# Optimization experiments

Hardware: AMD Instinct MI355X
Metric: run time of the kernel (lower is better)

## Reference

```python
import jax, jax.numpy as jnp
import numpy as np

N_NODES = 50000


def gcn_conv(x, W, b, src, dst, ew, n_nodes):
    """PyG GCNConv: out = D^{-1/2}(A + I)D^{-1/2} (x @ W) + b, A weighted by ew.

    Self loops (weight 1) are handled analytically instead of appending edges.
    """
    h = x @ W  # [N, out]
    # degree includes self-loop weight of 1
    deg = jax.ops.segment_sum(ew, dst, num_segments=n_nodes) + 1.0  # [N]
    dinv = jnp.where(deg > 0, jax.lax.rsqrt(deg), 0.0)
    norm = dinv[src] * ew * dinv[dst]  # [E]
    # message = norm * h[src], scatter-add to dst
    agg = jax.ops.segment_sum(h[src] * norm[:, None], dst, num_segments=n_nodes)
    # self-loop contribution: dinv[i] * 1 * dinv[i] * h[i]
    agg = agg + h * (dinv * dinv)[:, None]
    return agg + b


def setup_inputs() -> dict:
    key = jax.random.key(0)
    k = jax.random.split(key, 8)
    n, e, d_in, d_h = N_NODES, 600000, 128, 128
    x = jax.random.normal(k[0], (n, d_in), dtype=jnp.float32)
    edge_index = jax.random.randint(k[1], (2, e), 0, n, dtype=jnp.int64)
    edge_attr = jax.random.uniform(k[2], (e,), dtype=jnp.float32)
    s1 = 1.0 / np.sqrt(d_in)
    s2 = 1.0 / np.sqrt(d_h)
    W1 = jax.random.uniform(k[3], (d_in, d_h), jnp.float32, -s1, s1)
    b1 = jnp.zeros((d_h,), jnp.float32)
    W2 = jax.random.uniform(k[4], (d_h, d_h), jnp.float32, -s2, s2)
    b2 = jnp.zeros((d_h,), jnp.float32)
    return {"x": x, "edge_index": edge_index, "edge_attr": edge_attr,
            "W1": W1, "b1": b1, "W2": W2, "b2": b2}


def reference(x, edge_index, edge_attr, W1, b1, W2, b2):
    src, dst = edge_index[0], edge_index[1]
    h = gcn_conv(x, W1, b1, src, dst, edge_attr, N_NODES)
    h = jax.nn.relu(h)
    # dropout is identity in eval mode (deterministic reference)
    out = gcn_conv(h, W2, b2, src, dst, edge_attr, N_NODES)
    return out
```

## Files before the change

kernel.cpp:

```cpp
#include <hip/hip_runtime.h>
#include <stdint.h>

#define D 128
#define EPB2 1024
#define CSZ 128

typedef __bf16 bf16x8 __attribute__((ext_vector_type(8)));
typedef float f32x4 __attribute__((ext_vector_type(4)));

__device__ inline float bf2f(unsigned short u) {
    return __uint_as_float((unsigned)u << 16);
}
__device__ inline unsigned short f2bf(float f) {
    unsigned u = __float_as_uint(f);
    return (unsigned short)((u + 0x7FFF + ((u >> 16) & 1)) >> 16);
}

struct Params {
    const float* x; const int* ei; const float* ew;
    const float* W1; const float* b1; const float* W2; const float* b2;
    float* out;
    int N, E, C, B2n, gb, hb;
    unsigned short *Wt1, *Wt2;
    unsigned int* ctot; int* cbase; unsigned int* gcur;
    float* dinv; int* cnt; int* rowstart;
    int2* brec; int2* erec;
    unsigned short *Hbuf, *H2;
};


__device__ inline void dev_prep(int which, const Params& p) {
    const float* W = (which == 0) ? p.W1 : p.W2;
    unsigned short* Wt = (which == 0) ? p.Wt1 : p.Wt2;
    for (int i = threadIdx.x; i < 2048; i += 256) {
        int nn = i >> 4;
        int kc = (i & 15) << 3;
        ushort4 o0, o1;
        o0.x = f2bf(W[(kc + 0) * 128 + nn]); o0.y = f2bf(W[(kc + 1) * 128 + nn]);
        o0.z = f2bf(W[(kc + 2) * 128 + nn]); o0.w = f2bf(W[(kc + 3) * 128 + nn]);
        o1.x = f2bf(W[(kc + 4) * 128 + nn]); o1.y = f2bf(W[(kc + 5) * 128 + nn]);
        o1.z = f2bf(W[(kc + 6) * 128 + nn]); o1.w = f2bf(W[(kc + 7) * 128 + nn]);
        *(ushort4*)(Wt + nn * 128 + kc) = o0;
        *(ushort4*)(Wt + nn * 128 + kc + 4) = o1;
    }
}

__device__ inline void dev_hist2(int b, const Params& p, unsigned int* hist) {
    for (int i = threadIdx.x; i < p.C; i += 256) hist[i] = 0;
    __syncthreads();
    const int base = b * EPB2 + threadIdx.x;
#pragma unroll
    for (int k = 0; k < EPB2 / 256; ++k) {
        int e = base + k * 256;
        if (e < p.E) atomicAdd(&hist[((unsigned)p.ei[p.E + e]) >> 7], 1u);
    }
    __syncthreads();
    for (int i = threadIdx.x; i < p.C; i += 256) {
        unsigned v = hist[i];
        if (v) atomicAdd(&p.ctot[i], v);
    }
}

__device__ inline void dev_cscan(const Params& p, int* s) {
    const int tid = threadIdx.x;
    const int c0 = tid, c1 = tid + 256;
    s[c0] = (c0 < p.C) ? (int)p.ctot[c0] : 0;
    s[c1] = (c1 < p.C) ? (int)p.ctot[c1] : 0;
    __syncthreads();
    for (int off = 1; off < 512; off <<= 1) {
        int t0 = (c0 >= off) ? s[c0 - off] : 0;
        int t1 = (c1 >= off) ? s[c1 - off] : 0;
        __syncthreads();
        s[c0] += t0; s[c1] += t1;
        __syncthreads();
    }
    if (c0 < p.C) { int b0 = (c0 == 0) ? 0 : s[c0 - 1]; p.cbase[c0] = b0; p.gcur[c0] = (unsigned)b0; }
    if (c1 < p.C) { int b1 = s[c1 - 1]; p.cbase[c1] = b1; p.gcur[c1] = (unsigned)b1; }
    if (tid == 0) p.cbase[p.C] = p.E;
}

__device__ inline void dev_scat2(int b, const Params& p, unsigned int* a) {
    unsigned int* hcnt = a;
    unsigned int* hcur = a + 512;
    const int tid = threadIdx.x;
    for (int i = tid; i < p.C; i += 256) hcnt[i] = 0;
    __syncthreads();
    const int base = b * EPB2 + tid;
#pragma unroll
    for (int k = 0; k < EPB2 / 256; ++k) {
        int e = base + k * 256;
        if (e < p.E) atomicAdd(&hcnt[((unsigned)p.ei[p.E + e]) >> 7], 1u);
    }
    __syncthreads();
    for (int i = tid; i < p.C; i += 256) {
        unsigned c = hcnt[i];
        hcur[i] = c ? atomicAdd(&p.gcur[i], c) : 0u;
    }
    __syncthreads();
#pragma unroll
    for (int k = 0; k < EPB2 / 256; ++k) {
        int e = base + k * 256;
        if (e < p.E) {
            int s = p.ei[e];
            unsigned d = (unsigned)p.ei[p.E + e];
            float w = p.ew[e];
            int c = (int)(d >> 7);
            unsigned r = atomicAdd(&hcur[c], 1u);
            p.brec[r] = make_int2((int)((d << 16) | (unsigned)s), __float_as_int(w));
        }
    }
}

__device__ inline void dev_cbuild(int c, const Params& p, unsigned int* a, int cs, int ce) {
    unsigned int* hcnt = a;
    unsigned int* hdeg = a + CSZ;
    unsigned int* lsc  = a + 2 * CSZ;
    unsigned int* curs = a + 3 * CSZ;
    const int tid = threadIdx.x;
    if (tid < CSZ) { hcnt[tid] = 0; hdeg[tid] = 0; }
    __syncthreads();
    for (int i = cs + tid; i < ce; i += 256) {
        int2 r = p.brec[i];
        int local = (int)(((unsigned)r.x) >> 16) & (CSZ - 1);
        atomicAdd(&hcnt[local], 1u);
        atomicAdd(&hdeg[local], (unsigned)(__int_as_float(r.y) * 16777216.0f));
    }
    __syncthreads();
    if (tid < CSZ) lsc[tid] = hcnt[tid];
    __syncthreads();
    for (int off = 1; off < CSZ; off <<= 1) {
        unsigned t = (tid < CSZ && tid >= off) ? lsc[tid - off] : 0u;
        __syncthreads();
        if (tid < CSZ) lsc[tid] += t;
        __syncthreads();
    }
    if (tid < CSZ) {
        unsigned excl = lsc[tid] - hcnt[tid];
        curs[tid] = excl;
        int node = c * CSZ + tid;
        if (node < p.N) {
            p.rowstart[node] = cs + (int)excl;
            p.cnt[node] = (int)hcnt[tid];
            float deg = 1.0f + (float)hdeg[tid] * (1.0f / 16777216.0f);
            p.dinv[node] = rsqrtf(deg);
        }
    }
    __syncthreads();
    for (int i = cs + tid; i < ce; i += 256) {
        int2 r = p.brec[i];
        int local = (int)(((unsigned)r.x) >> 16) & (CSZ - 1);
        unsigned rk = atomicAdd(&curs[local], 1u);
        p.erec[cs + (int)rk] = make_int2(r.x & 0xFFFF, r.y);
    }
}

template <bool IN_BF16>
__device__ inline void mfma_body(unsigned short* sE,
                                 const void* __restrict__ Xv,
                                 const unsigned short* __restrict__ Wt,
                                 unsigned short* __restrict__ H, int n, int blk) {
    const int tid = threadIdx.x;
    const int row0 = blk * 64;
    const int lane = tid & 63;
    const int wv = tid >> 6;
    const int qm = lane & 15;
    const int quad = lane >> 4;

    const int arow = row0 + wv * 16 + qm;
    const int ar = (arow < n) ? arow : (n - 1);

    f32x4 acc[8];
#pragma unroll
    for (int i = 0; i < 8; ++i) acc[i] = (f32x4){0.f, 0.f, 0.f, 0.f};

#pragma unroll
    for (int kb = 0; kb < 4; ++kb) {
        const int koff = kb * 32 + quad * 8;
        bf16x8 a;
        if (IN_BF16) {
            a = *(const bf16x8*)((const unsigned short*)Xv + (size_t)ar * 128 + koff);
        } else {
            const float* Xf = (const float*)Xv + (size_t)ar * 128 + koff;
            float4 v0 = *(const float4*)(Xf);
            float4 v1 = *(const float4*)(Xf + 4);
            union { bf16x8 v; ushort4 u[2]; } cv;
            cv.u[0].x = f2bf(v0.x); cv.u[0].y = f2bf(v0.y);
            cv.u[0].z = f2bf(v0.z); cv.u[0].w = f2bf(v0.w);
            cv.u[1].x = f2bf(v1.x); cv.u[1].y = f2bf(v1.y);
            cv.u[1].z = f2bf(v1.z); cv.u[1].w = f2bf(v1.w);
            a = cv.v;
        }
#pragma unroll
        for (int n0 = 0; n0 < 8; ++n0) {
            bf16x8 b = *(const bf16x8*)(Wt + (n0 * 16 + qm) * 128 + koff);
            acc[n0] = __builtin_amdgcn_mfma_f32_16x16x32_bf16(a, b, acc[n0], 0, 0, 0);
        }
    }

#pragma unroll
    for (int n0 = 0; n0 < 8; ++n0)
#pragma unroll
        for (int r = 0; r < 4; ++r)
            sE[(wv * 16 + quad * 4 + r) * 136 + n0 * 16 + qm] = f2bf(acc[n0][r]);
    __syncthreads();

    const int row_in = lane >> 2;
    const int c0 = (lane & 3) * 4;
    const int grow = row0 + wv * 16 + row_in;
    if (grow < n) {
#pragma unroll
        for (int j = 0; j < 4; ++j)
            *(int4*)(H + (size_t)grow * 128 + (c0 + j) * 8) =
                *(const int4*)(&sE[(wv * 16 + row_in) * 136 + (c0 + j) * 8]);
    }
}

__device__ inline void gather1_to_lds(const Params& p, unsigned short* sA, int row0) {
    const int tid = threadIdx.x;
    const int lane8 = tid & 7;
    const int grp = tid >> 3;
    const ushort4* __restrict__ H4 = (const ushort4*)p.Hbuf;
#pragma unroll
    for (int pass = 0; pass < 2; ++pass) {
        const int local = pass * 32 + grp;
        const int node = row0 + local;
        unsigned short* dst = sA + local * 136 + lane8 * 16;
        if (node < p.N) {
            const int start = p.rowstart[node];
            const int m = p.cnt[node];
            const float di = p.dinv[node];
            const ushort4* Hrow = H4 + (size_t)node * 32 + lane8 * 4;
            float acc[16];
#pragma unroll
            for (int q = 0; q < 4; ++q) {
                ushort4 h = Hrow[q];
                acc[q * 4 + 0] = di * bf2f(h.x);
                acc[q * 4 + 1] = di * bf2f(h.y);
                acc[q * 4 + 2] = di * bf2f(h.z);
                acc[q * 4 + 3] = di * bf2f(h.w);
            }
            int j = 0;
            for (; j + 2 <= m; j += 2) {
                int2 e0 = p.erec[start + j];
                int2 e1 = p.erec[start + j + 1];
                float w0 = p.dinv[e0.x] * __int_as_float(e0.y);
                float w1 = p.dinv[e1.x] * __int_as_float(e1.y);
                const ushort4* V0 = H4 + (size_t)e0.x * 32 + lane8 * 4;
                const ushort4* V1 = H4 + (size_t)e1.x * 32 + lane8 * 4;
#pragma unroll
                for (int q = 0; q < 4; ++q) {
                    ushort4 v0 = V0[q], v1 = V1[q];
                    acc[q * 4 + 0] += w0 * bf2f(v0.x) + w1 * bf2f(v1.x);
                    acc[q * 4 + 1] += w0 * bf2f(v0.y) + w1 * bf2f(v1.y);
                    acc[q * 4 + 2] += w0 * bf2f(v0.z) + w1 * bf2f(v1.z);
                    acc[q * 4 + 3] += w0 * bf2f(v0.w) + w1 * bf2f(v1.w);
                }
            }
            if (j < m) {
                int2 e0 = p.erec[start + j];
                float w0 = p.dinv[e0.x] * __int_as_float(e0.y);
                const ushort4* V0 = H4 + (size_t)e0.x * 32 + lane8 * 4;
#pragma unroll
                for (int q = 0; q < 4; ++q) {
                    ushort4 v0 = V0[q];
                    acc[q * 4 + 0] += w0 * bf2f(v0.x);
                    acc[q * 4 + 1] += w0 * bf2f(v0.y);
                    acc[q * 4 + 2] += w0 * bf2f(v0.z);
                    acc[q * 4 + 3] += w0 * bf2f(v0.w);
                }
            }
            const float* bb = p.b1 + lane8 * 16;
#pragma unroll
            for (int q = 0; q < 4; ++q) {
                ushort4 o;
                o.x = f2bf(fmaxf(bb[q * 4 + 0] + di * acc[q * 4 + 0], 0.f));
                o.y = f2bf(fmaxf(bb[q * 4 + 1] + di * acc[q * 4 + 1], 0.f));
                o.z = f2bf(fmaxf(bb[q * 4 + 2] + di * acc[q * 4 + 2], 0.f));
                o.w = f2bf(fmaxf(bb[q * 4 + 3] + di * acc[q * 4 + 3], 0.f));
                *(ushort4*)(dst + q * 4) = o;
            }
        } else {
            ushort4 z = {0, 0, 0, 0};
#pragma unroll
            for (int q = 0; q < 4; ++q) *(ushort4*)(dst + q * 4) = z;
        }
    }
}

__device__ inline void gather2_body(const Params& p, const ushort4* __restrict__ H4,
                                    const float4* __restrict__ bias4,
                                    float4* __restrict__ OUT, int g) {
    const int lane = threadIdx.x & 31;
    const int node = g * 8 + (threadIdx.x >> 5);
    if (node >= p.N) return;
    const int start = p.rowstart[node];
    const int m = p.cnt[node];
    const float di = p.dinv[node];

    float4 b = bias4[lane];
    ushort4 h = H4[(size_t)node * 32 + lane];
    float ax = di * bf2f(h.x);
    float ay = di * bf2f(h.y);
    float az = di * bf2f(h.z);
    float aw = di * bf2f(h.w);

    int j = 0;
    for (; j + 4 <= m; j += 4) {
        const int base = start + j;
        int2 e0 = p.erec[base + 0], e1 = p.erec[base + 1];
        int2 e2 = p.erec[base + 2], e3 = p.erec[base + 3];
        float w0 = p.dinv[e0.x] * __int_as_float(e0.y);
        float w1 = p.dinv[e1.x] * __int_as_float(e1.y);
        float w2 = p.dinv[e2.x] * __int_as_float(e2.y);
        float w3 = p.dinv[e3.x] * __int_as_float(e3.y);
        ushort4 v0 = H4[(size_t)e0.x * 32 + lane];
        ushort4 v1 = H4[(size_t)e1.x * 32 + lane];
        ushort4 v2 = H4[(size_t)e2.x * 32 + lane];
        ushort4 v3 = H4[(size_t)e3.x * 32 + lane];
        ax += w0 * bf2f(v0.x); ay += w0 * bf2f(v0.y); az += w0 * bf2f(v0.z); aw += w0 * bf2f(v0.w);
        ax += w1 * bf2f(v1.x); ay += w1 * bf2f(v1.y); az += w1 * bf2f(v1.z); aw += w1 * bf2f(v1.w);
        ax += w2 * bf2f(v2.x); ay += w2 * bf2f(v2.y); az += w2 * bf2f(v2.z); aw += w2 * bf2f(v2.w);
        ax += w3 * bf2f(v3.x); ay += w3 * bf2f(v3.y); az += w3 * bf2f(v3.z); aw += w3 * bf2f(v3.w);
    }
    for (; j < m; ++j) {
        int2 er = p.erec[start + j];
        float w = p.dinv[er.x] * __int_as_float(er.y);
        ushort4 v = H4[(size_t)er.x * 32 + lane];
        ax += w * bf2f(v.x); ay += w * bf2f(v.y); az += w * bf2f(v.z); aw += w * bf2f(v.w);
    }
    float4 o;
    o.x = b.x + di * ax; o.y = b.y + di * ay;
    o.z = b.z + di * az; o.w = b.w + di * aw;
    OUT[(size_t)node * 32 + lane] = o;
}

__global__ __launch_bounds__(256, 4) void k_a0(Params p) {
    __shared__ __align__(16) unsigned int hist[512];
    if (blockIdx.x < 2) dev_prep(blockIdx.x, p);
    else dev_hist2(blockIdx.x - 2, p, hist);
}
__global__ __launch_bounds__(256, 4) void k_a1(Params p) {
    __shared__ __align__(16) char arena[64 * 136 * 2];
    if ((int)blockIdx.x < p.gb) mfma_body<false>((unsigned short*)arena, (const void*)p.x, p.Wt1, p.Hbuf, p.N, blockIdx.x);
    else dev_cscan(p, (int*)arena);
}
__global__ __launch_bounds__(256) void k_a2(Params p) {
    __shared__ unsigned int a[1024];
    dev_scat2(blockIdx.x, p, a);
}
__global__ __launch_bounds__(256) void k_a3(Params p) {
    __shared__ unsigned int a[4 * CSZ];
    dev_cbuild(blockIdx.x, p, a, p.cbase[blockIdx.x], p.cbase[blockIdx.x + 1]);
}
__global__ __launch_bounds__(256, 4) void k_a4(Params p) {
    __shared__ __align__(16) unsigned short sA[64 * 136];
    __shared__ __align__(16) unsigned short sE[64 * 136];
    const int row0 = blockIdx.x * 64;
    gather1_to_lds(p, sA, row0);
    __syncthreads();

    const int tid = threadIdx.x;
    const int lane = tid & 63;
    const int wv = tid >> 6;
    const int qm = lane & 15;
    const int quad = lane >> 4;

    f32x4 acc[8];
#pragma unroll
    for (int i = 0; i < 8; ++i) acc[i] = (f32x4){0.f, 0.f, 0.f, 0.f};

#pragma unroll
    for (int kb = 0; kb < 4; ++kb) {
        const int koff = kb * 32 + quad * 8;
        bf16x8 a = *(const bf16x8*)(sA + (wv * 16 + qm) * 136 + koff);
#pragma unroll
        for (int n0 = 0; n0 < 8; ++n0) {
            bf16x8 b = *(const bf16x8*)(p.Wt2 + (n0 * 16 + qm) * 128 + koff);
            acc[n0] = __builtin_amdgcn_mfma_f32_16x16x32_bf16(a, b, acc[n0], 0, 0, 0);
        }
    }

#pragma unroll
    for (int n0 = 0; n0 < 8; ++n0)
#pragma unroll
        for (int r = 0; r < 4; ++r)
            sE[(wv * 16 + quad * 4 + r) * 136 + n0 * 16 + qm] = f2bf(acc[n0][r]);
    __syncthreads();

    const int row_in = lane >> 2;
    const int c0 = (lane & 3) * 4;
    const int grow = row0 + wv * 16 + row_in;
    if (grow < p.N) {
#pragma unroll
        for (int j = 0; j < 4; ++j)
            *(int4*)(p.H2 + (size_t)grow * 128 + (c0 + j) * 8) =
                *(const int4*)(&sE[(wv * 16 + row_in) * 136 + (c0 + j) * 8]);
    }
}
__global__ __launch_bounds__(256) void k_a5(Params p) {
    gather2_body(p, (const ushort4*)p.H2, (const float4*)p.b2, (float4*)p.out, blockIdx.x);
}

extern "C" void kernel_launch(void* const* d_in, const int* in_sizes, int n_in,
                              void* d_out, int out_size, void* d_ws, size_t ws_size,
                              hipStream_t stream) {
    Params p;
    p.x  = (const float*)d_in[0];
    p.ei = (const int*)d_in[1];
    p.ew = (const float*)d_in[2];
    p.W1 = (const float*)d_in[3];
    p.b1 = (const float*)d_in[4];
    p.W2 = (const float*)d_in[5];
    p.b2 = (const float*)d_in[6];
    p.out = (float*)d_out;

    p.N = in_sizes[0] / D;
    p.E = in_sizes[2];
    p.C = (p.N + CSZ - 1) / CSZ;
    p.B2n = (p.E + EPB2 - 1) / EPB2;
    p.gb = (p.N + 63) / 64;
    p.hb = (p.N + 7) / 8;

    char* w = (char*)d_ws;
    auto alloc = [&](size_t bytes) {
        void* r = (void*)w;
        w += (bytes + 255) & ~(size_t)255;
        return r;
    };
    p.ctot     = (unsigned int*)alloc((size_t)p.C * 4);
    p.cbase    = (int*)alloc((size_t)(p.C + 1) * 4);
    p.gcur     = (unsigned int*)alloc((size_t)p.C * 4);
    p.dinv     = (float*)alloc((size_t)p.N * 4);
    p.cnt      = (int*)alloc((size_t)p.N * 4);
    p.rowstart = (int*)alloc((size_t)p.N * 4);
    p.brec     = (int2*)alloc((size_t)p.E * 8);
    p.erec     = (int2*)alloc((size_t)p.E * 8);
    p.Hbuf     = (unsigned short*)alloc((size_t)p.N * D * 2);
    p.H2       = (unsigned short*)alloc((size_t)p.N * D * 2);
    p.Wt1      = (unsigned short*)alloc(128 * 128 * 2);
    p.Wt2      = (unsigned short*)alloc(128 * 128 * 2);

    hipMemsetAsync(p.ctot, 0, (size_t)p.C * 4, stream);
    k_a0<<<2 + p.B2n, 256, 0, stream>>>(p);
    k_a1<<<p.gb + 1, 256, 0, stream>>>(p);
    k_a2<<<p.B2n, 256, 0, stream>>>(p);
    k_a3<<<p.C, 256, 0, stream>>>(p);
    k_a4<<<p.gb, 256, 0, stream>>>(p);
    k_a5<<<p.hb, 256, 0, stream>>>(p);
}
```

Measured before the change: 227.5 us.

## Pre-scale features by dinv in GEMM epilogue and split layer-2 gather from GEMM

```diff
diff --git a/kernel.cpp b/kernel.cpp
--- a/kernel.cpp
+++ b/kernel.cpp
@@ -23,9 +23,10 @@
     int N, E, C, B2n, gb, hb;
     unsigned short *Wt1, *Wt2;
     unsigned int* ctot; int* cbase; unsigned int* gcur;
+    float* deg;
     float* dinv; int* cnt; int* rowstart;
     int2* brec; int2* erec;
-    unsigned short *Hbuf, *H2;
+    unsigned short *Hbuf, *Abuf;
 };
 
 
@@ -52,7 +53,11 @@
 #pragma unroll
     for (int k = 0; k < EPB2 / 256; ++k) {
         int e = base + k * 256;
-        if (e < p.E) atomicAdd(&hist[((unsigned)p.ei[p.E + e]) >> 7], 1u);
+        if (e < p.E) {
+            unsigned d = (unsigned)p.ei[p.E + e];
+            atomicAdd(&hist[d >> 7], 1u);
+            atomicAdd(&p.deg[d], p.ew[e]);
+        }
     }
     __syncthreads();
     for (int i = threadIdx.x; i < p.C; i += 256) {
@@ -113,17 +118,15 @@
 
 __device__ inline void dev_cbuild(int c, const Params& p, unsigned int* a, int cs, int ce) {
     unsigned int* hcnt = a;
-    unsigned int* hdeg = a + CSZ;
-    unsigned int* lsc  = a + 2 * CSZ;
-    unsigned int* curs = a + 3 * CSZ;
+    unsigned int* lsc  = a + CSZ;
+    unsigned int* curs = a + 2 * CSZ;
     const int tid = threadIdx.x;
-    if (tid < CSZ) { hcnt[tid] = 0; hdeg[tid] = 0; }
+    if (tid < CSZ) hcnt[tid] = 0;
     __syncthreads();
     for (int i = cs + tid; i < ce; i += 256) {
         int2 r = p.brec[i];
         int local = (int)(((unsigned)r.x) >> 16) & (CSZ - 1);
         atomicAdd(&hcnt[local], 1u);
-        atomicAdd(&hdeg[local], (unsigned)(__int_as_float(r.y) * 16777216.0f));
     }
     __syncthreads();
     if (tid < CSZ) lsc[tid] = hcnt[tid];
@@ -141,8 +144,6 @@
         if (node < p.N) {
             p.rowstart[node] = cs + (int)excl;
             p.cnt[node] = (int)hcnt[tid];
-            float deg = 1.0f + (float)hdeg[tid] * (1.0f / 16777216.0f);
-            p.dinv[node] = rsqrtf(deg);
         }
     }
     __syncthreads();
@@ -154,11 +155,11 @@
     }
 }
 
-template <bool IN_BF16>
-__device__ inline void mfma_body(unsigned short* sE,
-                                 const void* __restrict__ Xv,
-                                 const unsigned short* __restrict__ Wt,
-                                 unsigned short* __restrict__ H, int n, int blk) {
+template <bool IN_BF16, bool FROM_DEG>
+__device__ inline void mfma_sc(unsigned short* sE, const Params& p,
+                               const void* __restrict__ Xv,
+                               const unsigned short* __restrict__ Wt,
+                               unsigned short* __restrict__ H, int n, int blk) {
     const int tid = threadIdx.x;
     const int row0 = blk * 64;
     const int lane = tid & 63;
@@ -197,11 +198,25 @@
         }
     }
 
+    const int crow = wv * 16 + quad * 4;
+    float di[4];
+#pragma unroll
+    for (int r = 0; r < 4; ++r) {
+        int rr = row0 + crow + r;
+        int rc = (rr < n) ? rr : (n - 1);
+        if (FROM_DEG) {
+            di[r] = rsqrtf(1.0f + p.deg[rc]);
+            if (qm == 0 && rr < n) p.dinv[rr] = di[r];
+        } else {
+            di[r] = p.dinv[rc];
+        }
+    }
+
 #pragma unroll
     for (int n0 = 0; n0 < 8; ++n0)
 #pragma unroll
         for (int r = 0; r < 4; ++r)
-            sE[(wv * 16 + quad * 4 + r) * 136 + n0 * 16 + qm] = f2bf(acc[n0][r]);
+            sE[(crow + r) * 136 + n0 * 16 + qm] = f2bf(acc[n0][r] * di[r]);
     __syncthreads();
 
     const int row_in = lane >> 2;
@@ -215,190 +230,99 @@
     }
 }
 
-__device__ inline void gather1_to_lds(const Params& p, unsigned short* sA, int row0) {
-    const int tid = threadIdx.x;
-    const int lane8 = tid & 7;
-    const int grp = tid >> 3;
-    const ushort4* __restrict__ H4 = (const ushort4*)p.Hbuf;
-#pragma unroll
-    for (int pass = 0; pass < 2; ++pass) {
-        const int local = pass * 32 + grp;
-        const int node = row0 + local;
-        unsigned short* dst = sA + local * 136 + lane8 * 16;
-        if (node < p.N) {
-            const int start = p.rowstart[node];
-            const int m = p.cnt[node];
-            const float di = p.dinv[node];
-            const ushort4* Hrow = H4 + (size_t)node * 32 + lane8 * 4;
-            float acc[16];
-#pragma unroll
-            for (int q = 0; q < 4; ++q) {
-                ushort4 h = Hrow[q];
-                acc[q * 4 + 0] = di * bf2f(h.x);
-                acc[q * 4 + 1] = di * bf2f(h.y);
-                acc[q * 4 + 2] = di * bf2f(h.z);
-                acc[q * 4 + 3] = di * bf2f(h.w);
-            }
-            int j = 0;
-            for (; j + 2 <= m; j += 2) {
-                int2 e0 = p.erec[start + j];
-                int2 e1 = p.erec[start + j + 1];
-                float w0 = p.dinv[e0.x] * __int_as_float(e0.y);
-                float w1 = p.dinv[e1.x] * __int_as_float(e1.y);
-                const ushort4* V0 = H4 + (size_t)e0.x * 32 + lane8 * 4;
-                const ushort4* V1 = H4 + (size_t)e1.x * 32 + lane8 * 4;
-#pragma unroll
-                for (int q = 0; q < 4; ++q) {
-                    ushort4 v0 = V0[q], v1 = V1[q];
-                    acc[q * 4 + 0] += w0 * bf2f(v0.x) + w1 * bf2f(v1.x);
-                    acc[q * 4 + 1] += w0 * bf2f(v0.y) + w1 * bf2f(v1.y);
-                    acc[q * 4 + 2] += w0 * bf2f(v0.z) + w1 * bf2f(v1.z);
-                    acc[q * 4 + 3] += w0 * bf2f(v0.w) + w1 * bf2f(v1.w);
-                }
-            }
-            if (j < m) {
-                int2 e0 = p.erec[start + j];
-                float w0 = p.dinv[e0.x] * __int_as_float(e0.y);
-                const ushort4* V0 = H4 + (size_t)e0.x * 32 + lane8 * 4;
-#pragma unroll
-                for (int q = 0; q < 4; ++q) {
-                    ushort4 v0 = V0[q];
-                    acc[q * 4 + 0] += w0 * bf2f(v0.x);
-                    acc[q * 4 + 1] += w0 * bf2f(v0.y);
-                    acc[q * 4 + 2] += w0 * bf2f(v0.z);
-                    acc[q * 4 + 3] += w0 * bf2f(v0.w);
-                }
-            }
-            const float* bb = p.b1 + lane8 * 16;
-#pragma unroll
-            for (int q = 0; q < 4; ++q) {
-                ushort4 o;
-                o.x = f2bf(fmaxf(bb[q * 4 + 0] + di * acc[q * 4 + 0], 0.f));
-                o.y = f2bf(fmaxf(bb[q * 4 + 1] + di * acc[q * 4 + 1], 0.f));
-                o.z = f2bf(fmaxf(bb[q * 4 + 2] + di * acc[q * 4 + 2], 0.f));
-                o.w = f2bf(fmaxf(bb[q * 4 + 3] + di * acc[q * 4 + 3], 0.f));
-                *(ushort4*)(dst + q * 4) = o;
-            }
-        } else {
-            ushort4 z = {0, 0, 0, 0};
-#pragma unroll
-            for (int q = 0; q < 4; ++q) *(ushort4*)(dst + q * 4) = z;
-        }
-    }
-}
-
-__device__ inline void gather2_body(const Params& p, const ushort4* __restrict__ H4,
-                                    const float4* __restrict__ bias4,
-                                    float4* __restrict__ OUT, int g) {
-    const int lane = threadIdx.x & 31;
-    const int node = g * 8 + (threadIdx.x >> 5);
+template <bool OUT_BF16, bool RELU>
+__device__ inline void gatherS(const Params& p, const unsigned short* __restrict__ Hs,
+                               const float* __restrict__ bias, void* __restrict__ OUTv, int g) {
+    const int lane = threadIdx.x & 15;
+    const int node = g * 16 + (threadIdx.x >> 4);
     if (node >= p.N) return;
     const int start = p.rowstart[node];
     const int m = p.cnt[node];
     const float di = p.dinv[node];
 
-    float4 b = bias4[lane];
-    ushort4 h = H4[(size_t)node * 32 + lane];
-    float ax = di * bf2f(h.x);
-    float ay = di * bf2f(h.y);
-    float az = di * bf2f(h.z);
-    float aw = di * bf2f(h.w);
-
+    const int4* __restrict__ H4 = (const int4*)Hs;
+    union U8 { int4 v; unsigned short u[8]; };
+    U8 s; s.v = H4[(size_t)node * 16 + lane];
+    float acc[8];
+#pragma unroll
+    for (int q = 0; q < 8; ++q) acc[q] = bf2f(s.u[q]);
+
+    const int2* __restrict__ er = p.erec + start;
     int j = 0;
     for (; j + 4 <= m; j += 4) {
-        const int base = start + j;
-        int2 e0 = p.erec[base + 0], e1 = p.erec[base + 1];
-        int2 e2 = p.erec[base + 2], e3 = p.erec[base + 3];
-        float w0 = p.dinv[e0.x] * __int_as_float(e0.y);
-        float w1 = p.dinv[e1.x] * __int_as_float(e1.y);
-        float w2 = p.dinv[e2.x] * __int_as_float(e2.y);
-        float w3 = p.dinv[e3.x] * __int_as_float(e3.y);
-        ushort4 v0 = H4[(size_t)e0.x * 32 + lane];
-        ushort4 v1 = H4[(size_t)e1.x * 32 + lane];
-        ushort4 v2 = H4[(size_t)e2.x * 32 + lane];
-        ushort4 v3 = H4[(size_t)e3.x * 32 + lane];
-        ax += w0 * bf2f(v0.x); ay += w0 * bf2f(v0.y); az += w0 * bf2f(v0.z); aw += w0 * bf2f(v0.w);
-        ax += w1 * bf2f(v1.x); ay += w1 * bf2f(v1.y); az += w1 * bf2f(v1.z); aw += w1 * bf2f(v1.w);
-        ax += w2 * bf2f(v2.x); ay += w2 * bf2f(v2.y); az += w2 * bf2f(v2.z); aw += w2 * bf2f(v2.w);
-        ax += w3 * bf2f(v3.x); ay += w3 * bf2f(v3.y); az += w3 * bf2f(v3.z); aw += w3 * bf2f(v3.w);
+        int2 e0 = er[j], e1 = er[j + 1], e2 = er[j + 2], e3 = er[j + 3];
+        U8 v0, v1, v2, v3;
+        v0.v = H4[(size_t)e0.x * 16 + lane];
+        v1.v = H4[(size_t)e1.x * 16 + lane];
+        v2.v = H4[(size_t)e2.x * 16 + lane];
+        v3.v = H4[(size_t)e3.x * 16 + lane];
+        float w0 = __int_as_float(e0.y), w1 = __int_as_float(e1.y);
+        float w2 = __int_as_float(e2.y), w3 = __int_as_float(e3.y);
+#pragma unroll
+        for (int q = 0; q < 8; ++q)
+            acc[q] += w0 * bf2f(v0.u[q]) + w1 * bf2f(v1.u[q]) +
+                      w2 * bf2f(v2.u[q]) + w3 * bf2f(v3.u[q]);
     }
     for (; j < m; ++j) {
-        int2 er = p.erec[start + j];
-        float w = p.dinv[er.x] * __int_as_float(er.y);
-        ushort4 v = H4[(size_t)er.x * 32 + lane];
-        ax += w * bf2f(v.x); ay += w * bf2f(v.y); az += w * bf2f(v.z); aw += w * bf2f(v.w);
-    }
-    float4 o;
-    o.x = b.x + di * ax; o.y = b.y + di * ay;
-    o.z = b.z + di * az; o.w = b.w + di * aw;
-    OUT[(size_t)node * 32 + lane] = o;
-}
-
-__global__ __launch_bounds__(256, 4) void k_a0(Params p) {
+        int2 e0 = er[j];
+        U8 v0; v0.v = H4[(size_t)e0.x * 16 + lane];
+        float w0 = __int_as_float(e0.y);
+#pragma unroll
+        for (int q = 0; q < 8; ++q) acc[q] += w0 * bf2f(v0.u[q]);
+    }
+
+    const float4 b0 = *(const float4*)(bias + lane * 8);
+    const float4 b1 = *(const float4*)(bias + lane * 8 + 4);
+    float o[8] = {b0.x, b0.y, b0.z, b0.w, b1.x, b1.y, b1.z, b1.w};
+#pragma unroll
+    for (int q = 0; q < 8; ++q) {
+        float v = o[q] + di * acc[q];
+        if (RELU) v = fmaxf(v, 0.f);
+        o[q] = v;
+    }
+    if (OUT_BF16) {
+        U8 ov;
+#pragma unroll
+        for (int q = 0; q < 8; ++q) ov.u[q] = f2bf(o[q]);
+        ((int4*)OUTv)[(size_t)node * 16 + lane] = ov.v;
+    } else {
+        float4 f0 = {o[0], o[1], o[2], o[3]};
+        float4 f1 = {o[4], o[5], o[6], o[7]};
+        float4* O = (float4*)OUTv;
+        O[(size_t)node * 32 + lane * 2] = f0;
+        O[(size_t)node * 32 + lane * 2 + 1] = f1;
+    }
+}
+
+__global__ __launch_bounds__(256, 4) void k_b0(Params p) {
     __shared__ __align__(16) unsigned int hist[512];
     if (blockIdx.x < 2) dev_prep(blockIdx.x, p);
     else dev_hist2(blockIdx.x - 2, p, hist);
 }
-__global__ __launch_bounds__(256, 4) void k_a1(Params p) {
+__global__ __launch_bounds__(256, 4) void k_b1(Params p) {
     __shared__ __align__(16) char arena[64 * 136 * 2];
-    if ((int)blockIdx.x < p.gb) mfma_body<false>((unsigned short*)arena, (const void*)p.x, p.Wt1, p.Hbuf, p.N, blockIdx.x);
-    else dev_cscan(p, (int*)arena);
-}
-__global__ __launch_bounds__(256) void k_a2(Params p) {
+    if ((int)blockIdx.x < p.gb)
+        mfma_sc<false, true>((unsigned short*)arena, p, (const void*)p.x, p.Wt1, p.Hbuf, p.N, blockIdx.x);
+    else
+        dev_cscan(p, (int*)arena);
+}
+__global__ __launch_bounds__(256) void k_b2(Params p) {
     __shared__ unsigned int a[1024];
     dev_scat2(blockIdx.x, p, a);
 }
-__global__ __launch_bounds__(256) void k_a3(Params p) {
-    __shared__ unsigned int a[4 * CSZ];
+__global__ __launch_bounds__(256) void k_b3(Params p) {
+    __shared__ unsigned int a[3 * CSZ];
     dev_cbuild(blockIdx.x, p, a, p.cbase[blockIdx.x], p.cbase[blockIdx.x + 1]);
 }
-__global__ __launch_bounds__(256, 4) void k_a4(Params p) {
-    __shared__ __align__(16) unsigned short sA[64 * 136];
-    __shared__ __align__(16) unsigned short sE[64 * 136];
-    const int row0 = blockIdx.x * 64;
-    gather1_to_lds(p, sA, row0);
-    __syncthreads();
-
-    const int tid = threadIdx.x;
-    const int lane = tid & 63;
-    const int wv = tid >> 6;
-    const int qm = lane & 15;
-    const int quad = lane >> 4;
-
-    f32x4 acc[8];
-#pragma unroll
-    for (int i = 0; i < 8; ++i) acc[i] = (f32x4){0.f, 0.f, 0.f, 0.f};
-
-#pragma unroll
-    for (int kb = 0; kb < 4; ++kb) {
-        const int koff = kb * 32 + quad * 8;
-        bf16x8 a = *(const bf16x8*)(sA + (wv * 16 + qm) * 136 + koff);
-#pragma unroll
-        for (int n0 = 0; n0 < 8; ++n0) {
-            bf16x8 b = *(const bf16x8*)(p.Wt2 + (n0 * 16 + qm) * 128 + koff);
-            acc[n0] = __builtin_amdgcn_mfma_f32_16x16x32_bf16(a, b, acc[n0], 0, 0, 0);
-        }
-    }
-
-#pragma unroll
-    for (int n0 = 0; n0 < 8; ++n0)
-#pragma unroll
-        for (int r = 0; r < 4; ++r)
-            sE[(wv * 16 + quad * 4 + r) * 136 + n0 * 16 + qm] = f2bf(acc[n0][r]);
-    __syncthreads();
-
-    const int row_in = lane >> 2;
-    const int c0 = (lane & 3) * 4;
-    const int grow = row0 + wv * 16 + row_in;
-    if (grow < p.N) {
-#pragma unroll
-        for (int j = 0; j < 4; ++j)
-            *(int4*)(p.H2 + (size_t)grow * 128 + (c0 + j) * 8) =
-                *(const int4*)(&sE[(wv * 16 + row_in) * 136 + (c0 + j) * 8]);
-    }
-}
-__global__ __launch_bounds__(256) void k_a5(Params p) {
-    gather2_body(p, (const ushort4*)p.H2, (const float4*)p.b2, (float4*)p.out, blockIdx.x);
+__global__ __launch_bounds__(256) void k_b4(Params p) {
+    gatherS<true, true>(p, p.Hbuf, p.b1, (void*)p.Abuf, blockIdx.x);
+}
+__global__ __launch_bounds__(256, 4) void k_b5(Params p) {
+    __shared__ __align__(16) char arena[64 * 136 * 2];
+    mfma_sc<true, false>((unsigned short*)arena, p, (const void*)p.Abuf, p.Wt2, p.Hbuf, p.N, blockIdx.x);
+}
+__global__ __launch_bounds__(256) void k_b6(Params p) {
+    gatherS<false, false>(p, p.Hbuf, p.b2, (void*)p.out, blockIdx.x);
 }
 
 extern "C" void kernel_launch(void* const* d_in, const int* in_sizes, int n_in,
@@ -419,7 +343,7 @@
     p.C = (p.N + CSZ - 1) / CSZ;
     p.B2n = (p.E + EPB2 - 1) / EPB2;
     p.gb = (p.N + 63) / 64;
-    p.hb = (p.N + 7) / 8;
+    p.hb = (p.N + 15) / 16;
 
     char* w = (char*)d_ws;
     auto alloc = [&](size_t bytes) {
@@ -428,6 +352,7 @@
         return r;
     };
     p.ctot     = (unsigned int*)alloc((size_t)p.C * 4);
+    p.deg      = (float*)alloc((size_t)p.N * 4);
     p.cbase    = (int*)alloc((size_t)(p.C + 1) * 4);
     p.gcur     = (unsigned int*)alloc((size_t)p.C * 4);
     p.dinv     = (float*)alloc((size_t)p.N * 4);
@@ -436,15 +361,18 @@
     p.brec     = (int2*)alloc((size_t)p.E * 8);
     p.erec     = (int2*)alloc((size_t)p.E * 8);
     p.Hbuf     = (unsigned short*)alloc((size_t)p.N * D * 2);
-    p.H2       = (unsigned short*)alloc((size_t)p.N * D * 2);
+    p.Abuf     = (unsigned short*)alloc((size_t)p.N * D * 2);
     p.Wt1      = (unsigned short*)alloc(128 * 128 * 2);
     p.Wt2      = (unsigned short*)alloc(128 * 128 * 2);
 
-    hipMemsetAsync(p.ctot, 0, (size_t)p.C * 4, stream);
-    k_a0<<<2 + p.B2n, 256, 0, stream>>>(p);
-    k_a1<<<p.gb + 1, 256, 0, stream>>>(p);
-    k_a2<<<p.B2n, 256, 0, stream>>>(p);
-    k_a3<<<p.C, 256, 0, stream>>>(p);
-    k_a4<<<p.gb, 256, 0, stream>>>(p);
-    k_a5<<<p.hb, 256, 0, stream>>>(p);
-}
+    size_t zspan = (size_t)((char*)p.deg - (char*)p.ctot) + (size_t)p.N * 4;
+    hipMemsetAsync(p.ctot, 0, zspan, stream);
+
+    k_b0<<<2 + p.B2n, 256, 0, stream>>>(p);
+    k_b1<<<p.gb + 1, 256, 0, stream>>>(p);
+    k_b2<<<p.B2n, 256, 0, stream>>>(p);
+    k_b3<<<p.C, 256, 0, stream>>>(p);
+    k_b4<<<p.hb, 256, 0, stream>>>(p);
+    k_b5<<<p.gb, 256, 0, stream>>>(p);
+    k_b6<<<p.hb, 256, 0, stream>>>(p);
+}
```

Measured after the change: 253.9 us. 11.6% more time.

## Use deterministic per-block histogram scan for edge bucketing and prescale H2 by dinv

Applied to the files above, without the earlier changes.

```diff
diff --git a/kernel.cpp b/kernel.cpp
--- a/kernel.cpp
+++ b/kernel.cpp
@@ -2,7 +2,7 @@
 #include <stdint.h>
 
 #define D 128
-#define EPB2 1024
+#define EPB 4096
 #define CSZ 128
 
 typedef __bf16 bf16x8 __attribute__((ext_vector_type(8)));
@@ -20,12 +20,12 @@
     const float* x; const int* ei; const float* ew;
     const float* W1; const float* b1; const float* W2; const float* b2;
     float* out;
-    int N, E, C, B2n, gb, hb;
+    int N, E, C, B1n, total, gb, hb, sb;
     unsigned short *Wt1, *Wt2;
-    unsigned int* ctot; int* cbase; unsigned int* gcur;
+    unsigned int* bh; int* ebase; int* bsums;
     float* dinv; int* cnt; int* rowstart;
     int2* brec; int2* erec;
-    unsigned short *Hbuf, *H2;
+    unsigned short *Hbuf, *Abuf;
 };
 
 
@@ -45,78 +45,79 @@
     }
 }
 
-__device__ inline void dev_hist2(int b, const Params& p, unsigned int* hist) {
+__device__ inline void dev_hist(int b, const Params& p, unsigned int* hist) {
     for (int i = threadIdx.x; i < p.C; i += 256) hist[i] = 0;
     __syncthreads();
-    const int base = b * EPB2 + threadIdx.x;
-#pragma unroll
-    for (int k = 0; k < EPB2 / 256; ++k) {
+    const int base = b * EPB + threadIdx.x;
+#pragma unroll
+    for (int k = 0; k < EPB / 256; ++k) {
         int e = base + k * 256;
         if (e < p.E) atomicAdd(&hist[((unsigned)p.ei[p.E + e]) >> 7], 1u);
     }
     __syncthreads();
-    for (int i = threadIdx.x; i < p.C; i += 256) {
-        unsigned v = hist[i];
-        if (v) atomicAdd(&p.ctot[i], v);
-    }
-}
-
-__device__ inline void dev_cscan(const Params& p, int* s) {
-    const int tid = threadIdx.x;
-    const int c0 = tid, c1 = tid + 256;
-    s[c0] = (c0 < p.C) ? (int)p.ctot[c0] : 0;
-    s[c1] = (c1 < p.C) ? (int)p.ctot[c1] : 0;
-    __syncthreads();
-    for (int off = 1; off < 512; off <<= 1) {
-        int t0 = (c0 >= off) ? s[c0 - off] : 0;
-        int t1 = (c1 >= off) ? s[c1 - off] : 0;
+    for (int i = threadIdx.x; i < p.C; i += 256) p.bh[(size_t)b * p.C + i] = hist[i];
+}
+
+__device__ inline void dev_scanA(int blk, const Params& p, int* tmp) {
+    const int tid = threadIdx.x;
+    const int i = blk * 256 + tid;
+    int v = 0;
+    if (i < p.total) {
+        int c = i / p.B1n;
+        int b = i - c * p.B1n;
+        v = (int)p.bh[(size_t)b * p.C + c];
+    }
+    tmp[tid] = v;
+    __syncthreads();
+    for (int off = 1; off < 256; off <<= 1) {
+        int t = (tid >= off) ? tmp[tid - off] : 0;
         __syncthreads();
-        s[c0] += t0; s[c1] += t1;
+        tmp[tid] += t;
         __syncthreads();
     }
-    if (c0 < p.C) { int b0 = (c0 == 0) ? 0 : s[c0 - 1]; p.cbase[c0] = b0; p.gcur[c0] = (unsigned)b0; }
-    if (c1 < p.C) { int b1 = s[c1 - 1]; p.cbase[c1] = b1; p.gcur[c1] = (unsigned)b1; }
-    if (tid == 0) p.cbase[p.C] = p.E;
-}
-
-__device__ inline void dev_scat2(int b, const Params& p, unsigned int* a) {
-    unsigned int* hcnt = a;
-    unsigned int* hcur = a + 512;
-    const int tid = threadIdx.x;
-    for (int i = tid; i < p.C; i += 256) hcnt[i] = 0;
-    __syncthreads();
-    const int base = b * EPB2 + tid;
-#pragma unroll
-    for (int k = 0; k < EPB2 / 256; ++k) {
-        int e = base + k * 256;
-        if (e < p.E) atomicAdd(&hcnt[((unsigned)p.ei[p.E + e]) >> 7], 1u);
-    }
-    __syncthreads();
-    for (int i = tid; i < p.C; i += 256) {
-        unsigned c = hcnt[i];
-        hcur[i] = c ? atomicAdd(&p.gcur[i], c) : 0u;
-    }
-    __syncthreads();
-#pragma unroll
-    for (int k = 0; k < EPB2 / 256; ++k) {
+    if (i < p.total) p.ebase[i] = tmp[tid] - v;
+    if (tid == 255) p.bsums[blk] = tmp[255];
+}
+
+__device__ inline void dev_scanB(int blk, const Params& p, int* sred) {
+    const int tid = threadIdx.x;
+    int v = (tid < blk) ? p.bsums[tid] : 0;
+#pragma unroll
+    for (int off = 32; off; off >>= 1) v += __shfl_down(v, off);
+    if ((tid & 63) == 0) sred[tid >> 6] = v;
+    __syncthreads();
+    int tot = sred[0] + sred[1] + sred[2] + sred[3];
+    int i = blk * 256 + tid;
+    if (i < p.total) p.ebase[i] += tot;
+}
+
+__device__ inline void dev_scat(int b, const Params& p, unsigned int* cur) {
+    for (int i = threadIdx.x; i < p.C; i += 256) cur[i] = 0;
+    __syncthreads();
+    const int base = b * EPB + threadIdx.x;
+#pragma unroll
+    for (int k = 0; k < EPB / 256; ++k) {
         int e = base + k * 256;
         if (e < p.E) {
             int s = p.ei[e];
             unsigned d = (unsigned)p.ei[p.E + e];
             float w = p.ew[e];
-            int c = (int)(d >> 7);
-            unsigned r = atomicAdd(&hcur[c], 1u);
-            p.brec[r] = make_int2((int)((d << 16) | (unsigned)s), __float_as_int(w));
-        }
-    }
-}
-
-__device__ inline void dev_cbuild(int c, const Params& p, unsigned int* a, int cs, int ce) {
+            int c = d >> 7;
+            unsigned r = atomicAdd(&cur[c], 1u);
+            int pos = p.ebase[c * p.B1n + b] + (int)r;
+            p.brec[pos] = make_int2((int)((d << 16) | (unsigned)s), __float_as_int(w));
+        }
+    }
+}
+
+__device__ inline void dev_cbuild(int c, const Params& p, unsigned int* a) {
     unsigned int* hcnt = a;
     unsigned int* hdeg = a + CSZ;
     unsigned int* lsc  = a + 2 * CSZ;
     unsigned int* curs = a + 3 * CSZ;
     const int tid = threadIdx.x;
+    const int cs = p.ebase[c * p.B1n];
+    const int ce = (c + 1 < p.C) ? p.ebase[(c + 1) * p.B1n] : p.E;
     if (tid < CSZ) { hcnt[tid] = 0; hdeg[tid] = 0; }
     __syncthreads();
     for (int i = cs + tid; i < ce; i += 256) {
@@ -299,20 +300,20 @@
 
     float4 b = bias4[lane];
     ushort4 h = H4[(size_t)node * 32 + lane];
-    float ax = di * bf2f(h.x);
-    float ay = di * bf2f(h.y);
-    float az = di * bf2f(h.z);
-    float aw = di * bf2f(h.w);
+    float ax = bf2f(h.x);
+    float ay = bf2f(h.y);
+    float az = bf2f(h.z);
+    float aw = bf2f(h.w);
 
     int j = 0;
     for (; j + 4 <= m; j += 4) {
         const int base = start + j;
         int2 e0 = p.erec[base + 0], e1 = p.erec[base + 1];
         int2 e2 = p.erec[base + 2], e3 = p.erec[base + 3];
-        float w0 = p.dinv[e0.x] * __int_as_float(e0.y);
-        float w1 = p.dinv[e1.x] * __int_as_float(e1.y);
-        float w2 = p.dinv[e2.x] * __int_as_float(e2.y);
-        float w3 = p.dinv[e3.x] * __int_as_float(e3.y);
+        float w0 = __int_as_float(e0.y);
+        float w1 = __int_as_float(e1.y);
+        float w2 = __int_as_float(e2.y);
+        float w3 = __int_as_float(e3.y);
         ushort4 v0 = H4[(size_t)e0.x * 32 + lane];
         ushort4 v1 = H4[(size_t)e1.x * 32 + lane];
         ushort4 v2 = H4[(size_t)e2.x * 32 + lane];
@@ -324,7 +325,7 @@
     }
     for (; j < m; ++j) {
         int2 er = p.erec[start + j];
-        float w = p.dinv[er.x] * __int_as_float(er.y);
+        float w = __int_as_float(er.y);
         ushort4 v = H4[(size_t)er.x * 32 + lane];
         ax += w * bf2f(v.x); ay += w * bf2f(v.y); az += w * bf2f(v.z); aw += w * bf2f(v.w);
     }
@@ -334,27 +335,30 @@
     OUT[(size_t)node * 32 + lane] = o;
 }
 
-__global__ __launch_bounds__(256, 4) void k_a0(Params p) {
+__global__ __launch_bounds__(256, 4) void k_f0(Params p) {
     __shared__ __align__(16) unsigned int hist[512];
     if (blockIdx.x < 2) dev_prep(blockIdx.x, p);
-    else dev_hist2(blockIdx.x - 2, p, hist);
-}
-__global__ __launch_bounds__(256, 4) void k_a1(Params p) {
+    else dev_hist(blockIdx.x - 2, p, hist);
+}
+__global__ __launch_bounds__(256, 4) void k_f1(Params p) {
     __shared__ __align__(16) char arena[64 * 136 * 2];
     if ((int)blockIdx.x < p.gb) mfma_body<false>((unsigned short*)arena, (const void*)p.x, p.Wt1, p.Hbuf, p.N, blockIdx.x);
-    else dev_cscan(p, (int*)arena);
-}
-__global__ __launch_bounds__(256) void k_a2(Params p) {
-    __shared__ unsigned int a[1024];
-    dev_scat2(blockIdx.x, p, a);
-}
-__global__ __launch_bounds__(256) void k_a3(Params p) {
+    else dev_scanA(blockIdx.x - p.gb, p, (int*)arena);
+}
+__global__ __launch_bounds__(256) void k_f2(Params p) {
+    __shared__ int sred[4];
+    dev_scanB(blockIdx.x, p, sred);
+}
+__global__ __launch_bounds__(256) void k_f3(Params p) {
+    __shared__ unsigned int cur[512];
+    dev_scat(blockIdx.x, p, cur);
+}
+__global__ __launch_bounds__(256) void k_f4(Params p) {
     __shared__ unsigned int a[4 * CSZ];
-    dev_cbuild(blockIdx.x, p, a, p.cbase[blockIdx.x], p.cbase[blockIdx.x + 1]);
-}
-__global__ __launch_bounds__(256, 4) void k_a4(Params p) {
+    dev_cbuild(blockIdx.x, p, a);
+}
+__global__ __launch_bounds__(256, 8) void k_g5(Params p) {
     __shared__ __align__(16) unsigned short sA[64 * 136];
-    __shared__ __align__(16) unsigned short sE[64 * 136];
     const int row0 = blockIdx.x * 64;
     gather1_to_lds(p, sA, row0);
     __syncthreads();
@@ -380,11 +384,21 @@
         }
     }
 
+    const int crow = wv * 16 + quad * 4;
+    float di[4];
+#pragma unroll
+    for (int r = 0; r < 4; ++r) {
+        int rr = row0 + crow + r;
+        int rc = (rr < p.N) ? rr : (p.N - 1);
+        di[r] = p.dinv[rc];
+    }
+
+    __syncthreads();
 #pragma unroll
     for (int n0 = 0; n0 < 8; ++n0)
 #pragma unroll
         for (int r = 0; r < 4; ++r)
-            sE[(wv * 16 + quad * 4 + r) * 136 + n0 * 16 + qm] = f2bf(acc[n0][r]);
+            sA[(crow + r) * 136 + n0 * 16 + qm] = f2bf(acc[n0][r] * di[r]);
     __syncthreads();
 
     const int row_in = lane >> 2;
@@ -393,12 +407,12 @@
     if (grow < p.N) {
 #pragma unroll
         for (int j = 0; j < 4; ++j)
-            *(int4*)(p.H2 + (size_t)grow * 128 + (c0 + j) * 8) =
-                *(const int4*)(&sE[(wv * 16 + row_in) * 136 + (c0 + j) * 8]);
-    }
-}
-__global__ __launch_bounds__(256) void k_a5(Params p) {
-    gather2_body(p, (const ushort4*)p.H2, (const float4*)p.b2, (float4*)p.out, blockIdx.x);
+            *(int4*)(p.Abuf + (size_t)grow * 128 + (c0 + j) * 8) =
+                *(const int4*)(&sA[(wv * 16 + row_in) * 136 + (c0 + j) * 8]);
+    }
+}
+__global__ __launch_bounds__(256) void k_g6(Params p) {
+    gather2_body(p, (const ushort4*)p.Abuf, (const float4*)p.b2, (float4*)p.out, blockIdx.x);
 }
 
 extern "C" void kernel_launch(void* const* d_in, const int* in_sizes, int n_in,
@@ -417,7 +431,9 @@
     p.N = in_sizes[0] / D;
     p.E = in_sizes[2];
     p.C = (p.N + CSZ - 1) / CSZ;
-    p.B2n = (p.E + EPB2 - 1) / EPB2;
+    p.B1n = (p.E + EPB - 1) / EPB;
+    p.total = p.C * p.B1n;
+    p.sb = (p.total + 255) / 256;
     p.gb = (p.N + 63) / 64;
     p.hb = (p.N + 7) / 8;
 
@@ -427,24 +443,24 @@
         w += (bytes + 255) & ~(size_t)255;
         return r;
     };
-    p.ctot     = (unsigned int*)alloc((size_t)p.C * 4);
-    p.cbase    = (int*)alloc((size_t)(p.C + 1) * 4);
-    p.gcur     = (unsigned int*)alloc((size_t)p.C * 4);
+    p.bh       = (unsigned int*)alloc((size_t)p.total * 4);
+    p.ebase    = (int*)alloc((size_t)p.total * 4);
+    p.bsums    = (int*)alloc(1024 * 4);
     p.dinv     = (float*)alloc((size_t)p.N * 4);
     p.cnt      = (int*)alloc((size_t)p.N * 4);
     p.rowstart = (int*)alloc((size_t)p.N * 4);
     p.brec     = (int2*)alloc((size_t)p.E * 8);
     p.erec     = (int2*)alloc((size_t)p.E * 8);
     p.Hbuf     = (unsigned short*)alloc((size_t)p.N * D * 2);
-    p.H2       = (unsigned short*)alloc((size_t)p.N * D * 2);
+    p.Abuf     = (unsigned short*)alloc((size_t)p.N * D * 2);
     p.Wt1      = (unsigned short*)alloc(128 * 128 * 2);
     p.Wt2      = (unsigned short*)alloc(128 * 128 * 2);
 
-    hipMemsetAsync(p.ctot, 0, (size_t)p.C * 4, stream);
-    k_a0<<<2 + p.B2n, 256, 0, stream>>>(p);
-    k_a1<<<p.gb + 1, 256, 0, stream>>>(p);
-    k_a2<<<p.B2n, 256, 0, stream>>>(p);
-    k_a3<<<p.C, 256, 0, stream>>>(p);
-    k_a4<<<p.gb, 256, 0, stream>>>(p);
-    k_a5<<<p.hb, 256, 0, stream>>>(p);
-}
+    k_f0<<<2 + p.B1n, 256, 0, stream>>>(p);
+    k_f1<<<p.gb + p.sb, 256, 0, stream>>>(p);
+    k_f2<<<p.sb, 256, 0, stream>>>(p);
+    k_f3<<<p.B1n, 256, 0, stream>>>(p);
+    k_f4<<<p.C, 256, 0, stream>>>(p);
+    k_g5<<<p.gb, 256, 0, stream>>>(p);
+    k_g6<<<p.hb, 256, 0, stream>>>(p);
+}
```

New measurement: 224.2 us. No clear change (-1.4%).
